# Kernel optimization log

Hardware: AMD Instinct MI355X
Metric: run time of the kernel (lower is better)

## Reference

```python
import jax, jax.numpy as jnp
import numpy as np

B, S, IN = 4, 4096, 2048
E, D, A, R = 16, 128, 128, 4  # num_experts, expert_vector_dim, attn_dim, mlp_rank
LN_EPS = 1e-5


def _ln2(x, g, b):
    # LayerNorm over the last two dims [E, D] jointly (torch nn.LayerNorm([E, D]))
    mu = x.mean(axis=(-2, -1), keepdims=True)
    var = ((x - mu) ** 2).mean(axis=(-2, -1), keepdims=True)
    return (x - mu) * jax.lax.rsqrt(var + LN_EPS) * g + b


def setup_inputs() -> dict:
    key = jax.random.key(0)
    ks = jax.random.split(key, 8)
    f32 = jnp.float32
    return {
        "hidden_states": jax.random.normal(ks[0], (B, S, IN), f32),
        "expert_embedding": jax.random.normal(ks[1], (E, D), f32) * 0.02,
        "ln_gamma": jnp.ones((E, D), f32),
        "ln_beta": jnp.zeros((E, D), f32),
        "Wv_w": jax.random.normal(ks[2], (E, IN), f32) * 0.02,
        "Wv_b": jnp.zeros((E,), f32),
        "mlp_w1": jax.random.normal(ks[3], (R, IN), f32) * 0.02,
        "mlp_b1": jnp.zeros((R,), f32),
        "mlp_w2": jax.random.normal(ks[4], (E * D, R), f32) * 0.02,
        "mlp_b2": jnp.zeros((E * D,), f32),
        "te_Wq": jax.random.normal(ks[5], (A, D), f32) * 0.05,
        "te_Wk": jax.random.normal(ks[6], (A, D), f32) * 0.05,
        "top_k": 2,
    }


def reference(hidden_states, expert_embedding, ln_gamma, ln_beta, Wv_w, Wv_b,
              mlp_w1, mlp_b1, mlp_w2, mlp_b2, te_Wq, te_Wk, top_k):
    # global expert vectors, layernormed over [E, D]: (E, D)
    ge = _ln2(expert_embedding[None, None], ln_gamma, ln_beta)[0, 0]
    # input gate = W_v(hidden): (B, S, E)
    input_gate = jnp.einsum('bsi,ei->bse', hidden_states, Wv_w) + Wv_b
    # TE mlp -> dynamic per-token expert vectors: (B, S, E, D)
    h = jax.nn.relu(jnp.einsum('bsi,ri->bsr', hidden_states, mlp_w1) + mlp_b1)
    dyn = (jnp.einsum('bsr,or->bso', h, mlp_w2) + mlp_b2).reshape(B, S, E, D)
    dyn = _ln2(dyn, ln_gamma, ln_beta)
    # attention-style routing: Q from dyn experts, K from global experts
    q = jnp.einsum('bsed,ad->bsea', dyn, te_Wq)     # (B, S, E, A)
    k = jnp.einsum('ed,ad->ea', ge, te_Wk)          # (E, A)
    scale = 1.0 / float(np.sqrt(A))
    sim = jax.nn.softmax(jnp.einsum('bsqa,ka->bsqk', q, k) * scale, axis=-1)
    gate = jnp.einsum('bsqk,bsk->bsq', sim, input_gate)
    rw = jax.nn.softmax(gate, axis=-1)              # (B, S, E)
    # top-k masking + sharpened softmax (temperature 0.1)
    vals, idx = jax.lax.top_k(rw, top_k)            # (B, S, k)
    oh = jax.nn.one_hot(idx, E, dtype=rw.dtype)     # (B, S, k, E)
    scattered = jnp.einsum('bske,bsk->bse', oh, vals)
    keep = oh.sum(axis=-2) > 0
    neg = jnp.finfo(rw.dtype).min
    masked = jnp.where(keep, scattered, neg)
    return jax.nn.softmax(masked / 0.1, axis=-1)
```

## Files before the change

### kernel.cpp

```cpp
#include <hip/hip_runtime.h>
#include <math.h>

#define NTOK   16384
#define INDIM  2048
#define NROWS  20
#define CHUNK  256

#define WS_PKT  0
#define WS_D1K  1024
#define WS_GQK  1280
#define WS_BQK  1536
#define WS_SCAL 1792
#define WS_TOT  1818

#define SIM_SCALE 0.08838834764831845f

#define LRED2_STRIDE 324
#define LRED    5440

__device__ __forceinline__ float fma4(float4 a, float4 b, float acc) {
    return fmaf(a.x, b.x, fmaf(a.y, b.y, fmaf(a.z, b.z, fmaf(a.w, b.w, acc))));
}

__device__ __forceinline__ void load_h(float4 h[4], const float* __restrict__ hb,
                                       int goff) {
    #pragma unroll
    for (int t = 0; t < 4; ++t)
        h[t] = *(const float4*)(hb + t * INDIM + goff);
}

__global__ __launch_bounds__(256) void hr_pre2(
    const float* __restrict__ ee, const float* __restrict__ gam,
    const float* __restrict__ bta, const float* __restrict__ w2,
    const float* __restrict__ b2, const float* __restrict__ wq,
    const float* __restrict__ wk, float* __restrict__ ws)
{
    const int tid  = threadIdx.x;
    const int bx   = blockIdx.x;
    const int lane = tid & 63;
    const int wave = tid >> 6;

    if (bx == 16) {
        __shared__ float sacc[26];
        if (tid < 26) sacc[tid] = 0.f;
        __syncthreads();
        float pa[26];
        #pragma unroll
        for (int j = 0; j < 26; ++j) pa[j] = 0.f;
        for (int i = tid; i < 2048; i += 256) {
            float b = b2[i];
            float4 w4 = *(const float4*)(w2 + i * 4);
            float wr[4] = {w4.x, w4.y, w4.z, w4.w};
            pa[0] += b;
            pa[1] += b * b;
            #pragma unroll
            for (int r = 0; r < 4; ++r) {
                pa[2 + r] += wr[r];
                pa[6 + r] += b * wr[r];
                #pragma unroll
                for (int r2 = 0; r2 < 4; ++r2) pa[10 + r * 4 + r2] += wr[r] * wr[r2];
            }
        }
        #pragma unroll
        for (int j = 0; j < 26; ++j) {
            float v = pa[j];
            v += __shfl_xor(v, 32); v += __shfl_xor(v, 16); v += __shfl_xor(v, 8);
            v += __shfl_xor(v, 4);  v += __shfl_xor(v, 2);  v += __shfl_xor(v, 1);
            if (lane == 0) atomicAdd(&sacc[j], v);
        }
        __syncthreads();
        if (tid < 26) ws[WS_SCAL + tid] = sacc[tid] * (1.f / 2048.f);
        return;
    }

    const int e2 = bx;
    __shared__ float sge[128];
    __shared__ float sK[128];
    __shared__ float sWqK[128];
    __shared__ float sred[8];

    float v8[8];
    float s = 0.f;
    #pragma unroll
    for (int j = 0; j < 8; ++j) { v8[j] = ee[tid + j * 256]; s += v8[j]; }
    s += __shfl_xor(s, 32); s += __shfl_xor(s, 16); s += __shfl_xor(s, 8);
    s += __shfl_xor(s, 4);  s += __shfl_xor(s, 2);  s += __shfl_xor(s, 1);
    if (lane == 0) sred[wave] = s;
    __syncthreads();
    const float mu = (sred[0] + sred[1] + sred[2] + sred[3]) * (1.f / 2048.f);
    float q = 0.f;
    #pragma unroll
    for (int j = 0; j < 8; ++j) { float d = v8[j] - mu; q += d * d; }
    q += __shfl_xor(q, 32); q += __shfl_xor(q, 16); q += __shfl_xor(q, 8);
    q += __shfl_xor(q, 4);  q += __shfl_xor(q, 2);  q += __shfl_xor(q, 1);
    if (lane == 0) sred[4 + wave] = q;
    __syncthreads();
    const float rsq = rsqrtf((sred[4] + sred[5] + sred[6] + sred[7]) * (1.f / 2048.f) + 1e-5f);

    if (tid < 128) {
        int idx = (e2 << 7) + tid;
        sge[tid] = (ee[idx] - mu) * rsq * gam[idx] + bta[idx];
    }
    __syncthreads();

    {
        int a = tid >> 1, half = tid & 1;
        const float* wr = wk + (a << 7) + (half << 6);
        const float* gg = sge + (half << 6);
        float acc = 0.f;
        #pragma unroll 8
        for (int j = 0; j < 64; ++j) acc = fmaf(gg[j], wr[j], acc);
        acc += __shfl_xor(acc, 1);
        if (half == 0) sK[a] = acc;
    }
    __syncthreads();

    {
        int d = tid >> 1, half = tid & 1;
        float acc = 0.f;
        #pragma unroll 8
        for (int j = 0; j < 64; ++j) {
            int a = (half << 6) + j;
            acc = fmaf(wq[(a << 7) + d], sK[a], acc);
        }
        acc += __shfl_xor(acc, 1);
        if (half == 0) sWqK[d] = acc;
    }
    __syncthreads();

    {
        int o = tid >> 2, qd = tid & 3;
        int r = o >> 4, e = o & 15;
        float acc = 0.f;
        #pragma unroll 8
        for (int j = 0; j < 32; ++j) {
            int d  = (qd << 5) + j;
            int ed = (e << 7) + d;
            acc = fmaf(w2[ed * 4 + r] * gam[ed], sWqK[d], acc);
        }
        acc += __shfl_xor(acc, 1);
        acc += __shfl_xor(acc, 2);
        if (qd == 0) ws[WS_PKT + (e2 << 6) + (r << 4) + e] = acc;
    }

    if (tid < 192) {
        int kind = tid >> 6;
        int e    = (tid >> 2) & 15;
        int qd   = tid & 3;
        float acc = 0.f;
        #pragma unroll 8
        for (int j = 0; j < 32; ++j) {
            int d  = (qd << 5) + j;
            int ed = (e << 7) + d;
            float w = sWqK[d];
            float t = (kind == 0) ? b2[ed] * gam[ed]
                    : (kind == 1) ? gam[ed]
                                  : bta[ed];
            acc = fmaf(t, w, acc);
        }
        acc += __shfl_xor(acc, 1);
        acc += __shfl_xor(acc, 2);
        if (qd == 0) ws[WS_D1K + (kind << 8) + (e2 << 4) + e] = acc;
    }
}

__global__ __launch_bounds__(256) void hr_main(
    const float* __restrict__ hidden, const float* __restrict__ wv,
    const float* __restrict__ wvb, const float* __restrict__ w1,
    const float* __restrict__ b1, const float* __restrict__ tab,
    float* __restrict__ out)
{
    __shared__ float lds[5760];

    const int tid  = threadIdx.x;
    const int wave = tid >> 6;
    const int lane = tid & 63;
    const int tok0 = (blockIdx.x << 4) + (wave << 2);
    const int l4   = lane << 2;
    const float* hb  = hidden + (size_t)tok0 * INDIM + l4;
    const float* wvl = wv + l4;
    const float* w1l = w1 + l4;

    float acc[NROWS][4];
    #pragma unroll
    for (int w = 0; w < NROWS; ++w) {
        acc[w][0] = 0.f; acc[w][1] = 0.f; acc[w][2] = 0.f; acc[w][3] = 0.f;
    }

    float4 h[4], hn[4];
    load_h(h, hb, 0);

    #pragma unroll 1
    for (int c = 0; c < 8; ++c) {
        const int goff = c << 8;
        float4 w[NROWS];
        #pragma unroll
        for (int r = 0; r < 16; ++r)
            w[r] = *(const float4*)(wvl + (r << 11) + goff);
        #pragma unroll
        for (int r = 0; r < 4; ++r)
            w[16 + r] = *(const float4*)(w1l + (r << 11) + goff);
        if (c < 7) load_h(hn, hb, goff + CHUNK);
        #pragma unroll
        for (int r = 0; r < NROWS; ++r) {
            #pragma unroll
            for (int t = 0; t < 4; ++t)
                acc[r][t] = fma4(h[t], w[r], acc[r][t]);
        }
        if (c < 7) {
            #pragma unroll
            for (int t = 0; t < 4; ++t) h[t] = hn[t];
        }
    }

    #pragma unroll
    for (int w = 0; w < NROWS; ++w) {
        #pragma unroll
        for (int t = 0; t < 4; ++t) {
            float v = acc[w][t];
            v += __shfl_xor(v, 32);
            v += __shfl_xor(v, 16);
            acc[w][t] = v;
        }
    }
    {
        const int q = lane >> 4, i = lane & 15;
        #pragma unroll
        for (int w = 0; w < NROWS; ++w) {
            if (q == w / 5) {
                #pragma unroll
                for (int t = 0; t < 4; ++t)
                    lds[((wave << 2) + t) * LRED2_STRIDE + (w << 4) + i] = acc[w][t];
            }
        }
    }
    __syncthreads();

    #pragma unroll
    for (int pp = 0; pp < 2; ++pp) {
        const int p = tid + pp * 256;
        if (p < 320) {
            const int w = p >> 4, tok = p & 15;
            const float4* rp = (const float4*)&lds[tok * LRED2_STRIDE + (w << 4)];
            float4 r0 = rp[0], r1 = rp[1], r2 = rp[2], r3 = rp[3];
            float s = (r0.x + r0.y + r0.z + r0.w) + (r1.x + r1.y + r1.z + r1.w)
                    + (r2.x + r2.y + r2.z + r2.w) + (r3.x + r3.y + r3.z + r3.w);
            lds[LRED + tok * 20 + w] = s;
        }
    }
    __syncthreads();

    const int tok = tid >> 4;
    const int e   = tid & 15;

    float ig[16];
    #pragma unroll
    for (int j = 0; j < 16; ++j) ig[j] = lds[LRED + tok * 20 + j] + wvb[j];
    float h2[4];
    #pragma unroll
    for (int r = 0; r < 4; ++r) h2[r] = fmaxf(lds[LRED + tok * 20 + 16 + r] + b1[r], 0.f);

    float muT = tab[WS_SCAL + 0];
    float e2m = tab[WS_SCAL + 1];
    #pragma unroll
    for (int r = 0; r < 4; ++r) {
        muT = fmaf(h2[r], tab[WS_SCAL + 2 + r], muT);
        e2m = fmaf(2.f * h2[r], tab[WS_SCAL + 6 + r], e2m);
        #pragma unroll
        for (int r2 = 0; r2 < 4; ++r2)
            e2m = fmaf(h2[r] * h2[r2], tab[WS_SCAL + 10 + r * 4 + r2], e2m);
    }
    const float var = e2m - muT * muT;
    const float rsq = rsqrtf(var + 1e-5f);

    float sv[16];
    #pragma unroll
    for (int e2 = 0; e2 < 16; ++e2) {
        float s = tab[WS_D1K + (e2 << 4) + e];
        s = fmaf(h2[0], tab[(e2 << 6) + e], s);
        s = fmaf(h2[1], tab[(e2 << 6) + 16 + e], s);
        s = fmaf(h2[2], tab[(e2 << 6) + 32 + e], s);
        s = fmaf(h2[3], tab[(e2 << 6) + 48 + e], s);
        s = fmaf(-muT, tab[WS_GQK + (e2 << 4) + e], s);
        sv[e2] = (rsq * s + tab[WS_BQK + (e2 << 4) + e]) * SIM_SCALE;
    }
    float mx = sv[0];
    #pragma unroll
    for (int e2 = 1; e2 < 16; ++e2) mx = fmaxf(mx, sv[e2]);
    float den = 0.f, gate = 0.f;
    #pragma unroll
    for (int e2 = 0; e2 < 16; ++e2) {
        float p = __expf(sv[e2] - mx);
        den += p;
        gate = fmaf(p, ig[e2], gate);
    }
    gate /= den;

    float gm = gate;
    gm = fmaxf(gm, __shfl_xor(gm, 1));
    gm = fmaxf(gm, __shfl_xor(gm, 2));
    gm = fmaxf(gm, __shfl_xor(gm, 4));
    gm = fmaxf(gm, __shfl_xor(gm, 8));
    float ex = __expf(gate - gm);
    float es = ex;
    es += __shfl_xor(es, 1);
    es += __shfl_xor(es, 2);
    es += __shfl_xor(es, 4);
    es += __shfl_xor(es, 8);
    const float rw = ex / es;

    float v1 = rw; int i1 = e;
    #pragma unroll
    for (int m = 1; m <= 8; m <<= 1) {
        float ov = __shfl_xor(v1, m);
        int   oi = __shfl_xor(i1, m);
        if (ov > v1 || (ov == v1 && oi < i1)) { v1 = ov; i1 = oi; }
    }
    float v2 = (e == i1) ? -INFINITY : rw; int i2 = e;
    #pragma unroll
    for (int m = 1; m <= 8; m <<= 1) {
        float ov = __shfl_xor(v2, m);
        int   oi = __shfl_xor(i2, m);
        if (ov > v2 || (ov == v2 && oi < i2)) { v2 = ov; i2 = oi; }
    }

    float oval = 0.f;
    if (e == i1 || e == i2) {
        float t = __expf((v2 - v1) * 10.f);
        oval = (e == i1) ? (1.f / (1.f + t)) : (t / (1.f + t));
    }
    out[(((size_t)blockIdx.x << 4) + tok) * 16 + e] = oval;
}

extern "C" void kernel_launch(void* const* d_in, const int* in_sizes, int n_in,
                              void* d_out, int out_size, void* d_ws, size_t ws_size,
                              hipStream_t stream)
{
    const float* hidden = (const float*)d_in[0];
    const float* ee     = (const float*)d_in[1];
    const float* gam    = (const float*)d_in[2];
    const float* bta    = (const float*)d_in[3];
    const float* wv     = (const float*)d_in[4];
    const float* wvb    = (const float*)d_in[5];
    const float* w1     = (const float*)d_in[6];
    const float* b1     = (const float*)d_in[7];
    const float* w2     = (const float*)d_in[8];
    const float* b2     = (const float*)d_in[9];
    const float* wq     = (const float*)d_in[10];
    const float* wk     = (const float*)d_in[11];
    float* out = (float*)d_out;
    float* ws  = (float*)d_ws;

    hipLaunchKernelGGL(hr_pre2, dim3(17), dim3(256), 0, stream,
                       ee, gam, bta, w2, b2, wq, wk, ws);
    hipLaunchKernelGGL(hr_main, dim3(NTOK / 16), dim3(256), 0, stream,
                       hidden, wv, wvb, w1, b1, ws, out);
}
```

Before: 250.2 us.

## Use single-wave blocks with double-buffered hidden loads and split weight phases

Each block of hr_main becomes one 64-thread wave handling 4 tokens, so the launch has 4x as many blocks and the LDS footprint shrinks. The chunk loop now double-buffers two hidden-state chunks (hA/hB) and prefetches two chunks ahead. Weight loads and FMAs are split into two 10-row halves separated by sched_barrier, which lowers peak weight-register pressure. The goal is better latency hiding and occupancy on the memory-bound GEMV. The cost is that weight rows get re-read per 4-token wave instead of being shared across the four waves of a block.

```diff
diff --git a/kernel.cpp b/kernel.cpp
--- a/kernel.cpp
+++ b/kernel.cpp
@@ -15,8 +15,8 @@
 
 #define SIM_SCALE 0.08838834764831845f
 
-#define LRED2_STRIDE 324
-#define LRED    5440
+#define LSCAT_T 320
+#define LRED    1280
 
 __device__ __forceinline__ float fma4(float4 a, float4 b, float acc) {
     return fmaf(a.x, b.x, fmaf(a.y, b.y, fmaf(a.z, b.z, fmaf(a.w, b.w, acc))));
@@ -27,6 +27,36 @@
     #pragma unroll
     for (int t = 0; t < 4; ++t)
         h[t] = *(const float4*)(hb + t * INDIM + goff);
+}
+
+template<int R0>
+__device__ __forceinline__ void half10(float acc[NROWS][4],
+                                       const float* __restrict__ wvl,
+                                       const float* __restrict__ w1l,
+                                       int goff, const float4 h[4]) {
+    float4 w[10];
+    #pragma unroll
+    for (int j = 0; j < 10; ++j) {
+        const int r = R0 + j;
+        const float* src = (r < 16) ? (wvl + (r << 11)) : (w1l + ((r - 16) << 11));
+        w[j] = *(const float4*)(src + goff);
+    }
+    #pragma unroll
+    for (int j = 0; j < 10; ++j) {
+        #pragma unroll
+        for (int t = 0; t < 4; ++t)
+            acc[R0 + j][t] = fma4(h[t], w[j], acc[R0 + j][t]);
+    }
+}
+
+__device__ __forceinline__ void chunk(float acc[NROWS][4],
+                                      const float* __restrict__ wvl,
+                                      const float* __restrict__ w1l,
+                                      int goff, const float4 h[4]) {
+    half10<0>(acc, wvl, w1l, goff, h);
+    __builtin_amdgcn_sched_barrier(0);
+    half10<10>(acc, wvl, w1l, goff, h);
+    __builtin_amdgcn_sched_barrier(0);
 }
 
 __global__ __launch_bounds__(256) void hr_pre2(
@@ -164,18 +194,16 @@
     }
 }
 
-__global__ __launch_bounds__(256) void hr_main(
+__global__ __launch_bounds__(64) void hr_main(
     const float* __restrict__ hidden, const float* __restrict__ wv,
     const float* __restrict__ wvb, const float* __restrict__ w1,
     const float* __restrict__ b1, const float* __restrict__ tab,
     float* __restrict__ out)
 {
-    __shared__ float lds[5760];
-
-    const int tid  = threadIdx.x;
-    const int wave = tid >> 6;
-    const int lane = tid & 63;
-    const int tok0 = (blockIdx.x << 4) + (wave << 2);
+    __shared__ float lds[1360];
+
+    const int lane = threadIdx.x;
+    const int tok0 = blockIdx.x << 2;
     const int l4   = lane << 2;
     const float* hb  = hidden + (size_t)tok0 * INDIM + l4;
     const float* wvl = wv + l4;
@@ -187,30 +215,17 @@
         acc[w][0] = 0.f; acc[w][1] = 0.f; acc[w][2] = 0.f; acc[w][3] = 0.f;
     }
 
-    float4 h[4], hn[4];
-    load_h(h, hb, 0);
+    float4 hA[4], hB[4];
+    load_h(hA, hb, 0);
+    load_h(hB, hb, CHUNK);
 
     #pragma unroll 1
-    for (int c = 0; c < 8; ++c) {
-        const int goff = c << 8;
-        float4 w[NROWS];
-        #pragma unroll
-        for (int r = 0; r < 16; ++r)
-            w[r] = *(const float4*)(wvl + (r << 11) + goff);
-        #pragma unroll
-        for (int r = 0; r < 4; ++r)
-            w[16 + r] = *(const float4*)(w1l + (r << 11) + goff);
-        if (c < 7) load_h(hn, hb, goff + CHUNK);
-        #pragma unroll
-        for (int r = 0; r < NROWS; ++r) {
-            #pragma unroll
-            for (int t = 0; t < 4; ++t)
-                acc[r][t] = fma4(h[t], w[r], acc[r][t]);
-        }
-        if (c < 7) {
-            #pragma unroll
-            for (int t = 0; t < 4; ++t) h[t] = hn[t];
-        }
+    for (int cc = 0; cc < 4; ++cc) {
+        const int g0 = cc << 9;
+        chunk(acc, wvl, w1l, g0, hA);
+        if (cc < 3) load_h(hA, hb, g0 + 512);
+        chunk(acc, wvl, w1l, g0 + 256, hB);
+        if (cc < 3) load_h(hB, hb, g0 + 768);
     }
 
     #pragma unroll
@@ -230,7 +245,7 @@
             if (q == w / 5) {
                 #pragma unroll
                 for (int t = 0; t < 4; ++t)
-                    lds[((wave << 2) + t) * LRED2_STRIDE + (w << 4) + i] = acc[w][t];
+                    lds[t * LSCAT_T + (w << 4) + i] = acc[w][t];
             }
         }
     }
@@ -238,20 +253,20 @@
 
     #pragma unroll
     for (int pp = 0; pp < 2; ++pp) {
-        const int p = tid + pp * 256;
-        if (p < 320) {
-            const int w = p >> 4, tok = p & 15;
-            const float4* rp = (const float4*)&lds[tok * LRED2_STRIDE + (w << 4)];
+        const int p = lane + (pp << 6);
+        if (p < 80) {
+            const int t = p / 20, w = p % 20;
+            const float4* rp = (const float4*)&lds[t * LSCAT_T + (w << 4)];
             float4 r0 = rp[0], r1 = rp[1], r2 = rp[2], r3 = rp[3];
             float s = (r0.x + r0.y + r0.z + r0.w) + (r1.x + r1.y + r1.z + r1.w)
                     + (r2.x + r2.y + r2.z + r2.w) + (r3.x + r3.y + r3.z + r3.w);
-            lds[LRED + tok * 20 + w] = s;
-        }
-    }
-    __syncthreads();
-
-    const int tok = tid >> 4;
-    const int e   = tid & 15;
+            lds[LRED + t * 20 + w] = s;
+        }
+    }
+    __syncthreads();
+
+    const int tok = lane >> 4;
+    const int e   = lane & 15;
 
     float ig[16];
     #pragma unroll
@@ -329,7 +344,7 @@
         float t = __expf((v2 - v1) * 10.f);
         oval = (e == i1) ? (1.f / (1.f + t)) : (t / (1.f + t));
     }
-    out[(((size_t)blockIdx.x << 4) + tok) * 16 + e] = oval;
+    out[(((size_t)blockIdx.x << 2) + tok) * 16 + e] = oval;
 }
 
 extern "C" void kernel_launch(void* const* d_in, const int* in_sizes, int n_in,
@@ -353,6 +368,6 @@
 
     hipLaunchKernelGGL(hr_pre2, dim3(17), dim3(256), 0, stream,
                        ee, gam, bta, w2, b2, wq, wk, ws);
-    hipLaunchKernelGGL(hr_main, dim3(NTOK / 16), dim3(256), 0, stream,
+    hipLaunchKernelGGL(hr_main, dim3(NTOK / 4), dim3(64), 0, stream,
                        hidden, wv, wvb, w1, b1, ws, out);
 }
```

Result: slower. 258.0 us (+3.1%).
